# Kernel optimization log

Measured on AMD Instinct MI355X. Metric: run time of the kernel, lower is better.

Reference implementation:

```python
import jax, jax.numpy as jnp
import numpy as np

HIDDEN = 768
HEADS = 12
HEAD_DIM = HIDDEN // HEADS  # 64


def setup_inputs() -> dict:
    key = jax.random.key(0)
    ks = jax.random.split(key, 7)
    B, S = 4, 2048
    std = 0.02
    return {
        "hidden_states": jax.random.normal(ks[0], (B, S, HIDDEN), dtype=jnp.float32),
        "attention_mask": jnp.zeros((B, 1, 1, S), dtype=jnp.float32),
        "Wq": jax.random.normal(ks[1], (HIDDEN, HIDDEN), dtype=jnp.float32) * std,
        "bq": jnp.zeros((HIDDEN,), dtype=jnp.float32),
        "Wk": jax.random.normal(ks[2], (HIDDEN, HIDDEN), dtype=jnp.float32) * std,
        "bk": jnp.zeros((HIDDEN,), dtype=jnp.float32),
        "Wv": jax.random.normal(ks[3], (HIDDEN, HIDDEN), dtype=jnp.float32) * std,
        "bv": jnp.zeros((HIDDEN,), dtype=jnp.float32),
    }


def _split_heads(x):
    # [B, S, HIDDEN] -> [B, H, S, D]
    B, S, _ = x.shape
    return x.reshape(B, S, HEADS, HEAD_DIM).transpose(0, 2, 1, 3)


def reference(hidden_states, attention_mask, Wq, bq, Wk, bk, Wv, bv):
    q = _split_heads(hidden_states @ Wq + bq)
    k = _split_heads(hidden_states @ Wk + bk)
    v = _split_heads(hidden_states @ Wv + bv)
    # [B, H, S, S] full score matrix (as in the original non-fused impl)
    scores = jnp.einsum("bhqd,bhkd->bhqk", q, k) / jnp.sqrt(
        jnp.asarray(HEAD_DIM, dtype=q.dtype)
    )
    scores = scores + attention_mask
    probs = jax.nn.softmax(scores, axis=-1)
    # dropout prob = 0.0 -> identity in eval
    ctx = jnp.einsum("bhqk,bhkd->bhqd", probs, v)
    B, H, S, D = ctx.shape
    return ctx.transpose(0, 2, 1, 3).reshape(B, S, H * D)
```

## Files before the change

kernel.cpp:

```cpp
#include <hip/hip_runtime.h>

typedef __bf16 bf16;
typedef __attribute__((ext_vector_type(8))) __bf16 bf16x8;
typedef __attribute__((ext_vector_type(4))) __bf16 bf16x4;
typedef __attribute__((ext_vector_type(4))) float f32x4;
typedef __attribute__((ext_vector_type(16))) float f32x16;
typedef __attribute__((ext_vector_type(4))) unsigned int u32x4;

#define DI __device__ __forceinline__

static constexpr int HID = 768;
static constexpr int SEQ = 2048;
static constexpr int NH  = 12;
static constexpr int HD  = 64;

DI void gload16(const void* g, void* l) {
  __builtin_amdgcn_global_load_lds(
      (const __attribute__((address_space(1))) void*)g,
      (__attribute__((address_space(3))) void*)l, 16, 0, 0);
}
DI int swz128(int row, int cb) { return row * 128 + (cb ^ ((row & 7) << 4)); }

DI unsigned cvtpk_bf16(float lo, float hi) {
  unsigned d;
  asm("v_cvt_pk_bf16_f32 %0, %1, %2" : "=v"(d) : "v"(lo), "v"(hi));
  return d;
}
DI void permswap(unsigned &a, unsigned &b) {
  asm("v_permlane32_swap_b32 %0, %1" : "+v"(a), "+v"(b));
}

__global__ void k_convert_x(const float* __restrict__ X, bf16* __restrict__ Xb, int n8) {
  int i = blockIdx.x * blockDim.x + threadIdx.x;
  if (i >= n8) return;
  const f32x4* Xv = (const f32x4*)X;
  f32x4 a = Xv[2 * i], b = Xv[2 * i + 1];
  bf16x8 o;
  o[0] = (bf16)a[0]; o[1] = (bf16)a[1]; o[2] = (bf16)a[2]; o[3] = (bf16)a[3];
  o[4] = (bf16)b[0]; o[5] = (bf16)b[1]; o[6] = (bf16)b[2]; o[7] = (bf16)b[3];
  *(bf16x8*)(Xb + (size_t)i * 8) = o;
}

__global__ void k_transpose_w(const float* __restrict__ Wq, const float* __restrict__ Wk,
                              const float* __restrict__ Wv, bf16* __restrict__ WT) {
  int z = blockIdx.z;
  const float* W = (z == 0) ? Wq : (z == 1) ? Wk : Wv;
  bf16* WTz = WT + (size_t)z * HID * HID;
  int k0 = blockIdx.x * 64, n0 = blockIdx.y * 64;
  __shared__ float t[64][65];
  int tt = threadIdx.x;
  for (int p = 0; p < 4; ++p) {
    int r = p * 16 + (tt >> 4), c4 = (tt & 15) * 4;
    f32x4 v = *(const f32x4*)(W + (size_t)(k0 + r) * HID + n0 + c4);
    t[c4 + 0][r] = v[0]; t[c4 + 1][r] = v[1]; t[c4 + 2][r] = v[2]; t[c4 + 3][r] = v[3];
  }
  __syncthreads();
  for (int p = 0; p < 4; ++p) {
    int rn = p * 16 + (tt >> 4), c4 = (tt & 15) * 4;
    bf16x4 o;
    o[0] = (bf16)t[rn][c4]; o[1] = (bf16)t[rn][c4 + 1];
    o[2] = (bf16)t[rn][c4 + 2]; o[3] = (bf16)t[rn][c4 + 3];
    *(bf16x4*)(WTz + (size_t)(n0 + rn) * HID + k0 + c4) = o;
  }
}

__global__ __launch_bounds__(256, 2)
void k_qkv_gemm(const bf16* __restrict__ Xb, const bf16* __restrict__ WT,
                const float* __restrict__ bq, const float* __restrict__ bk,
                const float* __restrict__ bv,
                bf16* __restrict__ Qb, bf16* __restrict__ Kb, bf16* __restrict__ VTb) {
  int z = blockIdx.z;
  const bf16* WTz = WT + (size_t)z * HID * HID;
  const float* bias = (z == 0) ? bq : (z == 1) ? bk : bv;

  int m0 = blockIdx.x * 128, n0 = blockIdx.y * 128;
  __shared__ char lds[32768];
  int w = threadIdx.x >> 6, l = threadIdx.x & 63;
  int wr = w >> 1, wc = w & 1;

  f32x4 acc[4][4] = {};

  for (int it = 0; it < HID / 64; ++it) {
    int k0 = it * 64;
    __syncthreads();
    for (int j = 0; j < 8; ++j) {
      int base = w * 8192 + j * 1024;
      int o = base + l * 16;
      const char* src;
      if (o < 16384) {
        int row = o >> 7;
        int cb = (o & 127) ^ ((row & 7) << 4);
        src = (const char*)(Xb + (size_t)(m0 + row) * HID + k0) + cb;
      } else {
        int o2 = o - 16384;
        int row = o2 >> 7;
        int cb = (o2 & 127) ^ ((row & 7) << 4);
        src = (const char*)(WTz + (size_t)(n0 + row) * HID + k0) + cb;
      }
      gload16(src, lds + base);
    }
    __syncthreads();

    for (int kk = 0; kk < 2; ++kk) {
      bf16x8 af[4], bfr[4];
      int cb = kk * 64 + ((l >> 4) << 4);
      for (int ms = 0; ms < 4; ++ms) {
        int row = wr * 64 + ms * 16 + (l & 15);
        af[ms] = *(const bf16x8*)(lds + swz128(row, cb));
      }
      for (int ns = 0; ns < 4; ++ns) {
        int row = wc * 64 + ns * 16 + (l & 15);
        bfr[ns] = *(const bf16x8*)(lds + 16384 + swz128(row, cb));
      }
      for (int ms = 0; ms < 4; ++ms)
        for (int ns = 0; ns < 4; ++ns)
          acc[ms][ns] = __builtin_amdgcn_mfma_f32_16x16x32_bf16(af[ms], bfr[ns], acc[ms][ns], 0, 0, 0);
    }
  }

  if (z == 2) {
    #pragma unroll
    for (int ns = 0; ns < 4; ++ns) {
      int col = n0 + wc * 64 + ns * 16 + (l & 15);
      float bvv = bias[col];
      int h = col >> 6, d = col & 63;
      #pragma unroll
      for (int ms = 0; ms < 4; ++ms) {
        int m = m0 + wr * 64 + ms * 16 + ((l >> 4) << 2);
        int bb = m >> 11, s = m & 2047;
        bf16x4 pk;
        #pragma unroll
        for (int r = 0; r < 4; ++r) pk[r] = (bf16)(acc[ms][ns][r] + bvv);
        *(bf16x4*)(VTb + (((size_t)(bb * NH + h) * HD + d) * SEQ + s)) = pk;
      }
    }
  } else {
    float scale = (z == 0) ? 0.125f : 1.0f;
    bf16* out = (z == 0) ? Qb : Kb;
    for (int ns = 0; ns < 4; ++ns) {
      int col = n0 + wc * 64 + ns * 16 + (l & 15);
      float bvv = bias[col];
      int h = col >> 6, d = col & 63;
      for (int ms = 0; ms < 4; ++ms) {
        for (int r = 0; r < 4; ++r) {
          int m = m0 + wr * 64 + ms * 16 + ((l >> 4) << 2) + r;
          int bb = m >> 11, s = m & 2047;
          float v = (acc[ms][ns][r] + bvv) * scale;
          out[(((size_t)(bb * NH + h) * SEQ + s) << 6) + d] = (bf16)v;
        }
      }
    }
  }
}

__global__ __launch_bounds__(256, 3)
void k_attn(const bf16* __restrict__ Qb, const bf16* __restrict__ Kb,
            const bf16* __restrict__ VTb, const float* __restrict__ mask,
            float* __restrict__ out) {
  __shared__ char lds[33280];
  constexpr int NT = SEQ / 64;
  int bh = blockIdx.x;
  int b = bh / NH, h = bh % NH;
  int q0 = blockIdx.y * 128;
  int w = threadIdx.x >> 6, l = threadIdx.x & 63;
  int q = l & 31, hi = l >> 5;
  const bf16* Qp = Qb + (size_t)bh * SEQ * HD;
  const char* Kbase = (const char*)(Kb + (size_t)bh * SEQ * HD);
  const char* VTbase = (const char*)(VTb + (size_t)bh * HD * SEQ);
  const float* mb = mask + (size_t)b * SEQ;

  bf16x8 qf[4];
  #pragma unroll
  for (int dstep = 0; dstep < 4; ++dstep)
    qf[dstep] = *(const bf16x8*)(Qp + (size_t)(q0 + w * 32 + q) * HD + dstep * 16 + hi * 8);

  f32x16 acc[2] = {};
  float psum = 0.f;

  int rbase = hi * 1024 + q * 16;

  auto stage = [&](int c, int kt) {
    const char* Kt = Kbase + (size_t)kt * 64 * 128;
    #pragma unroll
    for (int j = 0; j < 2; ++j) {
      int ch = w * 2 + j;
      gload16(Kt + l * 128 + ch * 16, lds + c * 16384 + ch * 1024);
    }
    #pragma unroll
    for (int j = 0; j < 2; ++j) {
      int ch = w * 2 + j;
      gload16(VTbase + (size_t)l * (SEQ * 2) + (size_t)kt * 128 + ch * 16,
              lds + c * 16384 + 8192 + ch * 1024);
    }
  };

  stage(0, 0);
  __syncthreads();

  int cur = 0;
  for (int kt = 0; kt < NT; ++kt) {
    if (kt + 1 < NT) stage(cur ^ 1, kt + 1);

    f32x4 mm[2][4];
    #pragma unroll
    for (int kh = 0; kh < 2; ++kh)
      #pragma unroll
      for (int blk = 0; blk < 4; ++blk)
        mm[kh][blk] = *(const f32x4*)(mb + kt * 64 + kh * 32 + blk * 8 + hi * 4);

    const char* Kl = lds + cur * 16384 + rbase;
    const char* Vl = lds + cur * 16384 + 8192 + rbase;

    #pragma unroll
    for (int kh = 0; kh < 2; ++kh) {
      bf16x8 kfh[4], vfk[4];
      #pragma unroll
      for (int dstep = 0; dstep < 4; ++dstep)
        kfh[dstep] = *(const bf16x8*)(Kl + dstep * 2048 + kh * 512);
      #pragma unroll
      for (int half = 0; half < 2; ++half)
        #pragma unroll
        for (int db = 0; db < 2; ++db)
          vfk[half * 2 + db] =
              *(const bf16x8*)(Vl + (kh * 2 + half) * 2048 + db * 512);

      f32x16 p;
      #pragma unroll
      for (int r = 0; r < 16; ++r) p[r] = mm[kh][r >> 2][r & 3];
      __builtin_amdgcn_s_setprio(1);
      #pragma unroll
      for (int dstep = 0; dstep < 4; ++dstep)
        p = __builtin_amdgcn_mfma_f32_32x32x16_bf16(kfh[dstep], qf[dstep], p, 0, 0, 0);
      __builtin_amdgcn_s_setprio(0);

      #pragma unroll
      for (int r = 0; r < 16; ++r) {
        float e = __expf(p[r]);
        p[r] = e;
        psum += e;
      }

      #pragma unroll
      for (int half = 0; half < 2; ++half) {
        int base = half * 8;
        unsigned a0 = cvtpk_bf16(p[base + 0], p[base + 1]);
        unsigned a1 = cvtpk_bf16(p[base + 2], p[base + 3]);
        unsigned a2 = cvtpk_bf16(p[base + 4], p[base + 5]);
        unsigned a3 = cvtpk_bf16(p[base + 6], p[base + 7]);
        permswap(a0, a2);
        permswap(a1, a3);
        u32x4 pk; pk[0] = a0; pk[1] = a1; pk[2] = a2; pk[3] = a3;
        bf16x8 PA = __builtin_bit_cast(bf16x8, pk);
        __builtin_amdgcn_s_setprio(1);
        #pragma unroll
        for (int db = 0; db < 2; ++db)
          acc[db] = __builtin_amdgcn_mfma_f32_32x32x16_bf16(PA, vfk[half * 2 + db], acc[db], 0, 0, 0);
        __builtin_amdgcn_s_setprio(0);
      }
    }

    __syncthreads();
    cur ^= 1;
  }

  float tot = psum + __shfl_xor(psum, 32);
  float* lsumL = (float*)(lds + 32768 + w * 128);
  if (l < 32) lsumL[l] = tot;
  __syncthreads();
  f32x4 lv[4];
  #pragma unroll
  for (int blk = 0; blk < 4; ++blk)
    lv[blk] = *(const f32x4*)(lsumL + blk * 8 + hi * 4);
  float inv[16];
  #pragma unroll
  for (int r = 0; r < 16; ++r) inv[r] = 1.0f / lv[r >> 2][r & 3];

  #pragma unroll
  for (int db = 0; db < 2; ++db)
    #pragma unroll
    for (int r = 0; r < 16; ++r) {
      int s = q0 + w * 32 + (r & 3) + 8 * (r >> 2) + 4 * hi;
      out[((size_t)(b * SEQ + s)) * HID + h * HD + db * 32 + q] = acc[db][r] * inv[r];
    }
}

extern "C" void kernel_launch(void* const* d_in, const int* in_sizes, int n_in,
                              void* d_out, int out_size, void* d_ws, size_t ws_size,
                              hipStream_t stream) {
  const float* X    = (const float*)d_in[0];
  const float* mask = (const float*)d_in[1];
  const float* Wq   = (const float*)d_in[2];
  const float* bq   = (const float*)d_in[3];
  const float* Wk   = (const float*)d_in[4];
  const float* bk   = (const float*)d_in[5];
  const float* Wv   = (const float*)d_in[6];
  const float* bv   = (const float*)d_in[7];
  float* out = (float*)d_out;
  char* ws = (char*)d_ws;

  const size_t SZ_XB = (size_t)8192 * HID * 2;
  const size_t SZ_WT = (size_t)3 * HID * HID * 2;
  const size_t SZ_M  = (size_t)4 * NH * SEQ * HD * 2;
  bf16* Xb  = (bf16*)(ws);
  bf16* WT  = (bf16*)(ws + SZ_XB);
  bf16* Qb  = (bf16*)(ws + SZ_XB + SZ_WT);
  bf16* Kb  = (bf16*)(ws + SZ_XB + SZ_WT + SZ_M);
  bf16* VTb = (bf16*)(ws + SZ_XB + SZ_WT + 2 * SZ_M);

  k_convert_x<<<3072, 256, 0, stream>>>(X, Xb, 8192 * HID / 8);
  k_transpose_w<<<dim3(12, 12, 3), 256, 0, stream>>>(Wq, Wk, Wv, WT);
  k_qkv_gemm<<<dim3(64, 6, 3), 256, 0, stream>>>(Xb, WT, bq, bk, bv, Qb, Kb, VTb);
  k_attn<<<dim3(48, 16), 256, 0, stream>>>(Qb, Kb, VTb, mask, out);
}
```

Measured before the change: 133.9 us.

## Store K and V^T in tile-blocked layout for contiguous attention tile loads

The projection epilogue now writes K and transposed V in a pre-tiled order: 64-key blocks whose 1 KiB chunks are already arranged the way the attention kernel's LDS layout expects. The attention stage can then copy each K/V tile with fully contiguous 16-byte global-to-LDS loads instead of row-strided gathers, with V^T rows previously SEQ*2 bytes apart. The cost is more scattered scalar writes of K in the projection epilogue, and the layouts of the two kernels are now tightly coupled.

```diff
diff --git a/kernel.cpp b/kernel.cpp
--- a/kernel.cpp
+++ b/kernel.cpp
@@ -131,12 +131,13 @@
         bf16x4 pk;
         #pragma unroll
         for (int r = 0; r < 4; ++r) pk[r] = (bf16)(acc[ms][ns][r] + bvv);
-        *(bf16x4*)(VTb + (((size_t)(bb * NH + h) * HD + d) * SEQ + s)) = pk;
-      }
-    }
-  } else {
-    float scale = (z == 0) ? 0.125f : 1.0f;
-    bf16* out = (z == 0) ? Qb : Kb;
+        size_t base = (size_t)(bb * NH + h) * HD * SEQ;
+        size_t idx = base + (size_t)(s >> 6) * 4096 + (size_t)((s >> 3) & 7) * 512
+                     + (size_t)d * 8 + (s & 7);
+        *(bf16x4*)(VTb + idx) = pk;
+      }
+    }
+  } else if (z == 1) {
     for (int ns = 0; ns < 4; ++ns) {
       int col = n0 + wc * 64 + ns * 16 + (l & 15);
       float bvv = bias[col];
@@ -145,8 +146,25 @@
         for (int r = 0; r < 4; ++r) {
           int m = m0 + wr * 64 + ms * 16 + ((l >> 4) << 2) + r;
           int bb = m >> 11, s = m & 2047;
-          float v = (acc[ms][ns][r] + bvv) * scale;
-          out[(((size_t)(bb * NH + h) * SEQ + s) << 6) + d] = (bf16)v;
+          float v = acc[ms][ns][r] + bvv;
+          size_t base = (size_t)(bb * NH + h) * SEQ * HD;
+          size_t idx = base + (size_t)(s >> 6) * 4096 + (size_t)(d >> 3) * 512
+                       + (size_t)(s & 63) * 8 + (d & 7);
+          Kb[idx] = (bf16)v;
+        }
+      }
+    }
+  } else {
+    for (int ns = 0; ns < 4; ++ns) {
+      int col = n0 + wc * 64 + ns * 16 + (l & 15);
+      float bvv = bias[col];
+      int h = col >> 6, d = col & 63;
+      for (int ms = 0; ms < 4; ++ms) {
+        for (int r = 0; r < 4; ++r) {
+          int m = m0 + wr * 64 + ms * 16 + ((l >> 4) << 2) + r;
+          int bb = m >> 11, s = m & 2047;
+          float v = (acc[ms][ns][r] + bvv) * 0.125f;
+          Qb[(((size_t)(bb * NH + h) * SEQ + s) << 6) + d] = (bf16)v;
         }
       }
     }
@@ -180,18 +198,16 @@
   int rbase = hi * 1024 + q * 16;
 
   auto stage = [&](int c, int kt) {
-    const char* Kt = Kbase + (size_t)kt * 64 * 128;
-    #pragma unroll
-    for (int j = 0; j < 2; ++j) {
-      int ch = w * 2 + j;
-      gload16(Kt + l * 128 + ch * 16, lds + c * 16384 + ch * 1024);
-    }
-    #pragma unroll
-    for (int j = 0; j < 2; ++j) {
-      int ch = w * 2 + j;
-      gload16(VTbase + (size_t)l * (SEQ * 2) + (size_t)kt * 128 + ch * 16,
-              lds + c * 16384 + 8192 + ch * 1024);
-    }
+    size_t t = (size_t)kt * 8192;
+    int off = w * 2048;
+    #pragma unroll
+    for (int j = 0; j < 2; ++j)
+      gload16(Kbase + t + off + j * 1024 + l * 16,
+              lds + c * 16384 + off + j * 1024);
+    #pragma unroll
+    for (int j = 0; j < 2; ++j)
+      gload16(VTbase + t + off + j * 1024 + l * 16,
+              lds + c * 16384 + 8192 + off + j * 1024);
   };
 
   stage(0, 0);
```

Result: faster. 120.6 us (-9.9%).
